# Optimization experiments

Measured on AMD Instinct MI355X. Metric: run time of the kernel, lower is better.

Reference implementation:

```python
import jax, jax.numpy as jnp
import numpy as np

N, B, E, H, G, L = 128, 2, 512, 1024, 50, 3
RBF_RADIUS = 12.0
AVG_LEN = 60.0


def _resmlp(h, Win, bin_, Wh, bh, Wout, bout):
    # input proj + activation, residual hidden blocks, linear head
    h = jax.nn.gelu(h @ Win + bin_, approximate=False)
    for i in range(Wh.shape[0]):  # fixed small number of layers
        h = h + jax.nn.gelu(h @ Wh[i] + bh[i], approximate=False)
    return h @ Wout + bout


def setup_inputs() -> dict:
    key = jax.random.key(0)
    ks = jax.random.split(key, 20)
    s_in = 1.0 / np.sqrt(3 * E)
    s_h = 1.0 / np.sqrt(H)
    s_g = 1.0 / np.sqrt(G)
    return {
        'x': jax.random.normal(ks[0], (N, B, E), jnp.float32),
        'dist': jax.random.uniform(ks[1], (N, N, B), jnp.float32),
        'vec_hat': jax.random.normal(ks[2], (N, N, B, 3), jnp.float32),
        'mask': jnp.ones((B, N), dtype=bool),
        'rbf_W': jax.random.normal(ks[3], (G, E), jnp.float32) * s_g,
        'rbf_b': jnp.zeros((E,), jnp.float32),
        'e_Win': jax.random.normal(ks[4], (3 * E, H), jnp.float32) * s_in,
        'e_bin': jnp.zeros((H,), jnp.float32),
        'e_Wh': jax.random.normal(ks[5], (L, H, H), jnp.float32) * s_h,
        'e_bh': jnp.zeros((L, H), jnp.float32),
        'e_Wout': jax.random.normal(ks[6], (H, 1), jnp.float32) * s_h,
        'e_bout': jnp.zeros((1,), jnp.float32),
        'f_Win': jax.random.normal(ks[7], (3 * E, H), jnp.float32) * s_in,
        'f_bin': jnp.zeros((H,), jnp.float32),
        'f_Wh': jax.random.normal(ks[8], (L, H, H), jnp.float32) * s_h,
        'f_bh': jnp.zeros((L, H), jnp.float32),
        'f_Wout': jax.random.normal(ks[9], (H, 1), jnp.float32) * s_h,
        'f_bout': jnp.zeros((1,), jnp.float32),
    }


def reference(x, dist, vec_hat, mask, rbf_W, rbf_b, e_Win, e_bin, e_Wh, e_bh,
              e_Wout, e_bout, f_Win, f_bin, f_Wh, f_bh, f_Wout, f_bout):
    # Gaussian RBF expansion + linear projection to embed_dim
    offset = jnp.linspace(0.0, RBF_RADIUS, G)
    coeff = -0.5 / (offset[1] - offset[0]) ** 2
    g = jnp.exp(coeff * (dist[..., None] - offset) ** 2)       # (N,N,B,G)
    rbf = g @ rbf_W + rbf_b                                    # (N,N,B,E)

    # all-pairs concat feature: [x_i, x_j, rbf_ij]  -> (N,N,B,3E)
    feat = jnp.concatenate([
        jnp.broadcast_to(x[:, None], rbf.shape),
        jnp.broadcast_to(x[None, :], rbf.shape),
        rbf,
    ], axis=-1)

    entries = (mask.T[:, None] & mask.T[None, :])[..., None].astype(feat.dtype)  # (N,N,B,1)

    energy_pairs = _resmlp(feat, e_Win, e_bin, e_Wh, e_bh, e_Wout, e_bout)       # (N,N,B,1)
    force_pairs = _resmlp(feat, f_Win, f_bin, f_Wh, f_bh, f_Wout, f_bout) * vec_hat  # (N,N,B,3)

    energy = (energy_pairs * entries).sum((0, 1)) / AVG_LEN ** 2  # (B,1)
    forces = (force_pairs * entries).sum(0) / AVG_LEN             # (N,B,3)
    # torch: forces.transpose(0,1)[mask]; mask is all-True here, so this is a reshape
    forces = jnp.swapaxes(forces, 0, 1).reshape(-1, 3)            # (B*N,3)
    return energy, forces
```

## Files before the change

### kernel.cpp

```cpp
#include <hip/hip_runtime.h>
#include <stdint.h>

typedef __bf16 bf16x8 __attribute__((ext_vector_type(8)));
typedef __bf16 bf16x4 __attribute__((ext_vector_type(4)));
typedef float  f32x4  __attribute__((ext_vector_type(4)));
typedef unsigned int u32;

__device__ __forceinline__ void gl_lds16(const void* gptr, void* lptr) {
    __builtin_amdgcn_global_load_lds(
        (const __attribute__((address_space(1))) u32*)gptr,
        (__attribute__((address_space(3))) u32*)lptr,
        16, 0, 0);
}

__device__ __forceinline__ float gelu_f(float x) {
    float u = 0.7978845608f * x * (1.0f + 0.044715f * x * x);
    float e = __expf(2.0f * u);
    float t = 1.0f - 2.0f / (e + 1.0f);
    return 0.5f * x * (1.0f + t);
}

#define MEMFENCE __asm__ __volatile__("" ::: "memory")

__global__ __launch_bounds__(256)
void prep_all(const float* __restrict__ dist, __bf16* __restrict__ G,
              const float* __restrict__ x, __bf16* __restrict__ xb,
              const float* __restrict__ rbfW, const float* __restrict__ rbf_b,
              __bf16* __restrict__ M1, float* __restrict__ out) {
    const int b = blockIdx.x;
    const int t = threadIdx.x;
    if (b < 1024) {
        const int row = b * 32 + (t >> 3);
        const int c0 = (t & 7) * 8;
        const float sp = 12.0f / 49.0f;
        const float coeff = -0.5f / (sp * sp);
        const float d = dist[row];
        bf16x8 v;
#pragma unroll
        for (int q = 0; q < 8; ++q) {
            const int k = c0 + q;
            float val;
            if (k < 50)       { float tt = d - (float)k * sp; val = __expf(coeff * tt * tt); }
            else if (k == 50) val = 1.0f;
            else              val = 0.0f;
            v[q] = (__bf16)val;
        }
        *(bf16x8*)(G + (size_t)row * 64 + c0) = v;
    } else if (b < 1152) {
        const int idx = (b - 1024) * 256 + t;
        float4 v = *(const float4*)(x + idx * 4);
        bf16x4 o;
        o[0] = (__bf16)v.x; o[1] = (__bf16)v.y; o[2] = (__bf16)v.z; o[3] = (__bf16)v.w;
        *(bf16x4*)(xb + idx * 4) = o;
    } else if (b < 1280) {
        const int tt = (b - 1152) * 256 + t;
        const int r = tt >> 8;
        const int c = (tt & 255) * 2;
        float v0 = 0.f, v1 = 0.f;
        if (r < 50)       { v0 = rbfW[r * 512 + c]; v1 = rbfW[r * 512 + c + 1]; }
        else if (r == 50) { v0 = rbf_b[c];          v1 = rbf_b[c + 1]; }
        M1[r * 512 + c] = (__bf16)v0;
        M1[r * 512 + c + 1] = (__bf16)v1;
    } else {
        const int i = (b - 1280) * 256 + t;
        if (i < 770) out[i] = 0.0f;
    }
}

__global__ __launch_bounds__(256)
void transpose_all(const float* __restrict__ eWin, const float* __restrict__ fWin,
                   __bf16* __restrict__ eWinT, __bf16* __restrict__ fWinT,
                   const float* __restrict__ eWh, const float* __restrict__ fWh,
                   __bf16* __restrict__ eWhT, __bf16* __restrict__ fWhT) {
    const int z = blockIdx.z;
    int K, branch, l;
    const float* src;
    __bf16* dst;
    if (z < 2) {
        K = 1536; branch = z; l = 0;
        src = branch ? fWin : eWin;
        dst = branch ? fWinT : eWinT;
    } else {
        K = 1024; const int zz = z - 2; branch = zz / 3; l = zz - branch * 3;
        src = (branch ? fWh : eWh) + (size_t)l * 1024 * 1024;
        dst = (branch ? fWhT : eWhT) + (size_t)l * 1024 * 1024;
    }
    const int Ncols = 1024;
    const int bk = blockIdx.x * 64;
    if (bk >= K) return;
    const int bn = blockIdx.y * 64;

    __shared__ float tile[64][65];
    const int tid = threadIdx.x;
    const int tr = tid >> 4;
    const int tc = (tid & 15) * 4;
#pragma unroll
    for (int p = 0; p < 4; ++p) {
        const int r = tr + p * 16;
        float4 v = *(const float4*)&src[(size_t)(bk + r) * Ncols + bn + tc];
        tile[r][tc] = v.x; tile[r][tc + 1] = v.y;
        tile[r][tc + 2] = v.z; tile[r][tc + 3] = v.w;
    }
    __syncthreads();
#pragma unroll
    for (int p = 0; p < 4; ++p) {
        const int rn = tr + p * 16;
        bf16x4 o;
        o[0] = (__bf16)tile[tc + 0][rn];
        o[1] = (__bf16)tile[tc + 1][rn];
        o[2] = (__bf16)tile[tc + 2][rn];
        o[3] = (__bf16)tile[tc + 3][rn];
        *(bf16x4*)&dst[(size_t)(bn + rn) * K + bk + tc] = o;
    }
}

template <int NK, int NBN, int MODE, bool DUAL, int MINW, bool SWZ>
__global__ __launch_bounds__(256, MINW)
void gemm_k(const __bf16* __restrict__ A0, const __bf16* __restrict__ A1,
            const __bf16* __restrict__ B0, const __bf16* __restrict__ B1,
            int lda, int ldb, int ldc,
            const float* __restrict__ bias0, const float* __restrict__ bias1,
            __bf16* __restrict__ C0, __bf16* __restrict__ C1,
            float* __restrict__ Cf0, float* __restrict__ Cf1,
            const float* __restrict__ P0, const float* __restrict__ P1,
            const float* __restrict__ wout0, const float* __restrict__ wout1,
            float* __restrict__ dot0, float* __restrict__ dot1) {
    constexpr int NBS = (NBN == 16) ? 4 : (NBN == 8) ? 3 : 0;
    __shared__ __align__(16) __bf16 As[3][128 * 32];
    __shared__ __align__(16) __bf16 Bs[3][128 * 32];

    const int tid = threadIdx.x;
    int bn, bm, branch = 0;
    if constexpr (SWZ) {
        const int x = blockIdx.x & 7;
        const int slot = blockIdx.x >> 3;
        bn = slot & (NBN - 1);
        int grp = x + ((slot >> NBS) << 3);
        if constexpr (DUAL) {
            const int half = (gridDim.x >> NBS) >> 1;
            branch = (grp >= half);
            if (branch) grp -= half;
        }
        bm = grp;
    } else {
        int f2 = blockIdx.x;
        if constexpr (DUAL) {
            const int half = gridDim.x >> 1;
            branch = (f2 >= half);
            if (branch) f2 -= half;
        }
        bn = f2 & (NBN - 1);
        bm = f2 >> NBS;
    }
    const int w = tid >> 6;
    const int lane = tid & 63;

    const __bf16* Ab = (DUAL && branch) ? A1 : A0;
    const __bf16* Bb = (DUAL && branch) ? B1 : B0;

    const int r0 = tid >> 2;
    const int s0 = tid & 3;
    const char* gA0 = (const char*)Ab + (size_t)(bm * 128 + r0) * lda + s0 * 16;
    const char* gA1 = gA0 + (size_t)64 * lda;
    const char* gB0 = (const char*)Bb + (size_t)(bn * 128 + r0) * ldb + s0 * 16;
    const char* gB1 = gB0 + (size_t)64 * ldb;

    char* lA0 = (char*)&As[0][0] + w * 1024;
    char* lA1 = (char*)&As[1][0] + w * 1024;
    char* lA2 = (char*)&As[2][0] + w * 1024;
    char* lB0 = (char*)&Bs[0][0] + w * 1024;
    char* lB1 = (char*)&Bs[1][0] + w * 1024;
    char* lB2 = (char*)&Bs[2][0] + w * 1024;

    const int wm = (w >> 1) & 1;
    const int wn = w & 1;
    const int lm = lane & 15;
    const int ko = (lane >> 4) << 3;
    const int fo = (wm * 64 + lm) * 32 + ko;
    const int go = (wn * 64 + lm) * 32 + ko;
    const __bf16* pA0 = &As[0][0] + fo;
    const __bf16* pA1 = &As[1][0] + fo;
    const __bf16* pA2 = &As[2][0] + fo;
    const __bf16* pB0 = &Bs[0][0] + go;
    const __bf16* pB1 = &Bs[1][0] + go;
    const __bf16* pB2 = &Bs[2][0] + go;

    f32x4 acc[4][4];
    const f32x4 zero = {0.0f, 0.0f, 0.0f, 0.0f};
#pragma unroll
    for (int i = 0; i < 4; ++i)
#pragma unroll
        for (int j = 0; j < 4; ++j) acc[i][j] = zero;

    auto stage = [&](int buf) {
        char* la = (buf == 0) ? lA0 : (buf == 1) ? lA1 : lA2;
        char* lb = (buf == 0) ? lB0 : (buf == 1) ? lB1 : lB2;
        gl_lds16(gA0, la); gl_lds16(gA1, la + 4096);
        gl_lds16(gB0, lb); gl_lds16(gB1, lb + 4096);
        gA0 += 64; gA1 += 64; gB0 += 64; gB1 += 64;
    };
    auto compute = [&](int buf) {
        const __bf16* pa = (buf == 0) ? pA0 : (buf == 1) ? pA1 : pA2;
        const __bf16* pb = (buf == 0) ? pB0 : (buf == 1) ? pB1 : pB2;
        bf16x8 af[4], bfg[4];
#pragma unroll
        for (int i = 0; i < 4; ++i) {
            af[i]  = *(const bf16x8*)(pa + i * 512);
            bfg[i] = *(const bf16x8*)(pb + i * 512);
        }
#pragma unroll
        for (int mi = 0; mi < 4; ++mi)
#pragma unroll
            for (int ni = 0; ni < 4; ++ni)
                acc[mi][ni] = __builtin_amdgcn_mfma_f32_16x16x32_bf16(
                    af[mi], bfg[ni], acc[mi][ni], 0, 0, 0);
    };
    auto iterstep = [&](int cbuf, int sbuf) {
        MEMFENCE;
        __builtin_amdgcn_s_waitcnt(0xF74);
        __builtin_amdgcn_s_barrier();
        MEMFENCE;
        compute(cbuf);
        MEMFENCE;
        stage(sbuf);
        MEMFENCE;
    };

    stage(0);
    stage(1);
    constexpr int NIT = NK - 2;
    constexpr int NG = NIT / 3;
    constexpr int NR = NIT % 3;
    for (int g = 0; g < NG; ++g) {
        iterstep(0, 2);
        iterstep(1, 0);
        iterstep(2, 1);
    }
    if constexpr (NR >= 1) iterstep(0, 2);
    if constexpr (NR >= 2) iterstep(1, 0);
    MEMFENCE;
    __builtin_amdgcn_s_waitcnt(0xF74);
    __builtin_amdgcn_s_barrier();
    MEMFENCE;
    compute((NK - 2) % 3);
    MEMFENCE;
    __builtin_amdgcn_s_waitcnt(0xF70);
    __builtin_amdgcn_s_barrier();
    MEMFENCE;
    compute((NK - 1) % 3);

    const int col0 = bn * 128 + wn * 64 + lm;
    const int row0 = bm * 128 + wm * 64 + ((lane >> 4) << 2);
    const int ldaE = lda >> 1;

    float rowdot[16];
    if constexpr (MODE == 1) {
#pragma unroll
        for (int q = 0; q < 16; ++q) rowdot[q] = 0.0f;
    }

    const bool side = (MODE == 2) && (bn >= 8);
    const float* bp = (MODE == 2) ? (side ? bias1 : bias0)
                                  : ((DUAL && branch) ? bias1 : bias0);
    __bf16* Cout = (MODE == 2) ? (side ? C1 : C0)
                               : ((DUAL && branch) ? C1 : C0);
    const float* woutb = (MODE == 1) ? ((DUAL && branch) ? wout1 : wout0) : nullptr;

#pragma unroll
    for (int ni = 0; ni < 4; ++ni) {
        const int gn = col0 + ni * 16;
        const int gnl = (MODE == 2) ? (gn & 1023) : gn;
        float bv = 0.0f;
        if constexpr (MODE <= 2) bv = bp[gnl];
        float wv = 0.0f;
        if constexpr (MODE == 1) wv = woutb[gn];

        float res[16];
        if constexpr (MODE == 0 || MODE == 1) {
#pragma unroll
            for (int mi = 0; mi < 4; ++mi)
#pragma unroll
                for (int rr = 0; rr < 4; ++rr)
                    res[mi * 4 + rr] =
                        (float)Ab[(size_t)(row0 + mi * 16 + rr) * ldaE + gn];
        } else if constexpr (MODE == 2) {
#pragma unroll
            for (int mi = 0; mi < 4; ++mi)
#pragma unroll
                for (int rr = 0; rr < 4; ++rr) {
                    const int gm = row0 + mi * 16 + rr;
                    const int p0row = ((gm >> 8) << 1) | (gm & 1);
                    const int p1row = gm & 255;
                    res[mi * 4 + rr] = P0[(size_t)p0row * 2048 + gn]
                                     + P1[(size_t)p1row * 2048 + gn];
                }
        }
        MEMFENCE;

#pragma unroll
        for (int mi = 0; mi < 4; ++mi) {
#pragma unroll
            for (int rr = 0; rr < 4; ++rr) {
                const int gm = row0 + mi * 16 + rr;
                const float a = acc[mi][ni][rr];
                if constexpr (MODE == 0) {
                    float v = gelu_f(a + bv) + res[mi * 4 + rr];
                    Cout[(size_t)gm * ldc + gn] = (__bf16)v;
                } else if constexpr (MODE == 1) {
                    float v = gelu_f(a + bv) + res[mi * 4 + rr];
                    rowdot[mi * 4 + rr] += v * wv;
                } else if constexpr (MODE == 2) {
                    float v = a + bv + res[mi * 4 + rr];
                    Cout[(size_t)gm * ldc + gnl] = (__bf16)gelu_f(v);
                } else if constexpr (MODE == 3) {
                    float* Cfw = (DUAL && branch) ? Cf1 : Cf0;
                    Cfw[(size_t)gm * ldc + gn] = a;
                } else {
                    C0[(size_t)gm * ldc + gn] = (__bf16)a;
                }
            }
        }
    }

    if constexpr (MODE == 1) {
#pragma unroll
        for (int s = 1; s < 16; s <<= 1)
#pragma unroll
            for (int q = 0; q < 16; ++q) rowdot[q] += __shfl_xor(rowdot[q], s);
        if (lm == 0) {
            float* dotb = (DUAL && branch) ? dot1 : dot0;
            float* dp = dotb + (size_t)(bn * 2 + wn) * 32768 + row0;
#pragma unroll
            for (int q = 0; q < 16; ++q)
                dp[(q >> 2) * 16 + (q & 3)] = rowdot[q];
        }
    }
}

#define WBAR(imm) do { MEMFENCE; __builtin_amdgcn_s_waitcnt(imm); \
                       __builtin_amdgcn_s_barrier(); MEMFENCE; } while (0)

template <int MODE, bool DUAL, int NBN, int NT, int LDA, int LDB>
__global__ __launch_bounds__(256, 2)
void gemm256(const __bf16* __restrict__ A0, const __bf16* __restrict__ A1,
             const __bf16* __restrict__ B0, const __bf16* __restrict__ B1,
             const float* __restrict__ bias0, const float* __restrict__ bias1,
             __bf16* __restrict__ C0, __bf16* __restrict__ C1,
             const float* __restrict__ wout0, const float* __restrict__ wout1,
             float* __restrict__ dot0, float* __restrict__ dot1,
             const float* __restrict__ P0, const float* __restrict__ P1) {
    constexpr int NBS = (NBN == 16) ? 4 : (NBN == 8) ? 3 : 2;
    __shared__ __align__(16) char ldsbuf[2 * 24576];

    const int tid = threadIdx.x;
    const int nxg = gridDim.x >> 3;
    const int id = (blockIdx.x & 7) * nxg + (blockIdx.x >> 3);
    const int bn = id & (NBN - 1);
    int rest = id >> NBS;
    int branch = 0;
    if constexpr (DUAL) { branch = rest >> 7; rest &= 127; }
    const int bm = rest;

    const __bf16* __restrict__ Ab = (DUAL && branch) ? A1 : A0;
    const __bf16* __restrict__ Bb = (DUAL && branch) ? B1 : B0;

    const int w = tid >> 6;
    const int lane = tid & 63;

    const int srow = tid >> 2;
    const int scol = ((tid & 3) << 4) ^ (((tid >> 3) & 3) << 4);
    const char* gA = (const char*)Ab + (size_t)(bm * 256 + srow) * LDA + scol;
    const char* gB = (const char*)Bb + (size_t)(bn * 128 + srow) * LDB + scol;

    auto stageT = [&](int kt, int buf) {
        const size_t ko = (size_t)kt * 64;
        char* d = ldsbuf + buf * 24576 + w * 1024;
        gl_lds16(gA + ko,             d);
        gl_lds16(gA + ko +  64 * LDA, d + 4096);
        gl_lds16(gA + ko + 128 * LDA, d + 8192);
        gl_lds16(gA + ko + 192 * LDA, d + 12288);
        gl_lds16(gB + ko,             d + 16384);
        gl_lds16(gB + ko +  64 * LDB, d + 20480);
    };

    const int wm = w >> 1, wn = w & 1;
    const int lm = lane & 15, lq = lane >> 4;
    const int swz = ((lm >> 1) & 3) << 4;
    const int rA = (wm * 128 + lm) * 64 + ((lq * 16) ^ swz);
    const int rB = 16384 + (wn * 64 + lm) * 64 + ((lq * 16) ^ swz);

    f32x4 acc[4][8];
    const f32x4 zero = {0.0f, 0.0f, 0.0f, 0.0f};
#pragma unroll
    for (int i = 0; i < 4; ++i)
#pragma unroll
        for (int j = 0; j < 8; ++j) acc[i][j] = zero;

    auto body2 = [&](int kt, int buf, bool dostage) {
        const char* Lb = ldsbuf + buf * 24576;
        MEMFENCE;
        bf16x8 a[8], b[4];
#pragma unroll
        for (int ni = 0; ni < 4; ++ni)
            b[ni] = *(const bf16x8*)(Lb + rB + ni * 1024);
#pragma unroll
        for (int mi = 0; mi < 8; ++mi)
            a[mi] = *(const bf16x8*)(Lb + rA + mi * 1024);
        MEMFENCE;
        __builtin_amdgcn_s_waitcnt(0xC07F);
        MEMFENCE;
        __builtin_amdgcn_s_barrier();
        MEMFENCE;
        if (dostage) stageT(kt + 2, buf);
        MEMFENCE;
        __builtin_amdgcn_s_setprio(1);
#pragma unroll
        for (int ni = 0; ni < 4; ++ni)
#pragma unroll
            for (int mi = 0; mi < 8; ++mi)
                acc[ni][mi] = __builtin_amdgcn_mfma_f32_16x16x32_bf16(
                    b[ni], a[mi], acc[ni][mi], 0, 0, 0);
        __builtin_amdgcn_s_setprio(0);
    };

    if constexpr (NT == 32) {
        stageT(0, 0);
        stageT(1, 1);
        for (int g = 0; g < 15; ++g) {
            WBAR(0xF76); body2(2 * g + 0, 0, true);
            WBAR(0xF76); body2(2 * g + 1, 1, true);
        }
        WBAR(0xF76); body2(30, 0, false);
        WBAR(0xF70); body2(31, 1, false);
    } else {
        stageT(0, 0);
        stageT(1, 1);
        WBAR(0xF76); body2(0, 0, false);
        WBAR(0xF70); body2(1, 1, false);
    }

    const int rowb = bm * 256 + wm * 128 + lm;
    const int nbase = bn * 128 + wn * 64 + lq * 4;

    if constexpr (MODE == 2) {
        const bool side = (bn >= (NBN >> 1));
        const float* __restrict__ bp = side ? bias1 : bias0;
        __bf16* __restrict__ Cw = side ? C1 : C0;
        const int nloc = nbase & 1023;
        f32x4 bv[4], p0v[4];
        const size_t p0base = (size_t)((bm << 1) | (lm & 1)) * 2048;
#pragma unroll
        for (int ni = 0; ni < 4; ++ni) {
            bv[ni]  = *(const f32x4*)&bp[nloc + ni * 16];
            p0v[ni] = *(const f32x4*)&P0[p0base + nbase + ni * 16];
        }
#pragma unroll
        for (int mi = 0; mi < 8; ++mi) {
            const int p1row = wm * 128 + mi * 16 + lm;
            f32x4 p1v[4];
#pragma unroll
            for (int ni = 0; ni < 4; ++ni)
                p1v[ni] = *(const f32x4*)&P1[(size_t)p1row * 2048 + nbase + ni * 16];
            MEMFENCE;
            const size_t rb = (size_t)(rowb + mi * 16) * 1024;
#pragma unroll
            for (int ni = 0; ni < 4; ++ni) {
                bf16x4 o;
#pragma unroll
                for (int r = 0; r < 4; ++r)
                    o[r] = (__bf16)gelu_f(acc[ni][mi][r] + bv[ni][r] +
                                          p0v[ni][r] + p1v[ni][r]);
                *(bf16x4*)&Cw[rb + nloc + ni * 16] = o;
            }
        }
        return;
    }

    const float* __restrict__ bp = (DUAL && branch) ? bias1 : bias0;
    f32x4 bv[4];
#pragma unroll
    for (int ni = 0; ni < 4; ++ni)
        bv[ni] = *(const f32x4*)&bp[nbase + ni * 16];

    if constexpr (MODE == 0) {
        __bf16* __restrict__ Cw = (DUAL && branch) ? C1 : C0;
#pragma unroll
        for (int mi = 0; mi < 8; ++mi) {
            const size_t rb = (size_t)(rowb + mi * 16) * 1024;
            bf16x4 res[4];
#pragma unroll
            for (int ni = 0; ni < 4; ++ni)
                res[ni] = *(const bf16x4*)&Ab[rb + nbase + ni * 16];
            MEMFENCE;
#pragma unroll
            for (int ni = 0; ni < 4; ++ni) {
                bf16x4 o;
#pragma unroll
                for (int r = 0; r < 4; ++r)
                    o[r] = (__bf16)(gelu_f(acc[ni][mi][r] + bv[ni][r]) +
                                    (float)res[ni][r]);
                *(bf16x4*)&Cw[rb + nbase + ni * 16] = o;
            }
        }
    } else if constexpr (MODE == 1) {
        const float* __restrict__ wb = (DUAL && branch) ? wout1 : wout0;
        f32x4 wv[4];
#pragma unroll
        for (int ni = 0; ni < 4; ++ni)
            wv[ni] = *(const f32x4*)&wb[nbase + ni * 16];
        float rd[8];
#pragma unroll
        for (int q = 0; q < 8; ++q) rd[q] = 0.0f;
#pragma unroll
        for (int mi = 0; mi < 8; ++mi) {
            const size_t rb = (size_t)(rowb + mi * 16) * 1024;
            bf16x4 res[4];
#pragma unroll
            for (int ni = 0; ni < 4; ++ni)
                res[ni] = *(const bf16x4*)&Ab[rb + nbase + ni * 16];
            MEMFENCE;
#pragma unroll
            for (int ni = 0; ni < 4; ++ni)
#pragma unroll
                for (int r = 0; r < 4; ++r) {
                    float v = gelu_f(acc[ni][mi][r] + bv[ni][r]) +
                              (float)res[ni][r];
                    rd[mi] += v * wv[ni][r];
                }
        }
#pragma unroll
        for (int mi = 0; mi < 8; ++mi) {
            rd[mi] += __shfl_xor(rd[mi], 16);
            rd[mi] += __shfl_xor(rd[mi], 32);
        }
        if (lq == 0) {
            float* __restrict__ db = (DUAL && branch) ? dot1 : dot0;
            float* dp = db + (size_t)(bn * 2 + wn) * 32768 + bm * 256 + wm * 128;
#pragma unroll
            for (int mi = 0; mi < 8; ++mi)
                dp[mi * 16 + lm] = rd[mi];
        }
    }
}

__global__ __launch_bounds__(128)
void finalize(const float* __restrict__ dot_e, const float* __restrict__ dot_f,
              const float* __restrict__ eb, const float* __restrict__ fb,
              const float* __restrict__ vec, float* __restrict__ out) {
    const int bj = blockIdx.x;
    const int bb = bj >> 7, jj = bj & 127;
    const int i = threadIdx.x;
    const int m = (i * 128 + jj) * 2 + bb;
    float e = eb[0], f = fb[0];
#pragma unroll
    for (int s = 0; s < 16; ++s) {
        e += dot_e[(size_t)s * 32768 + m];
        f += dot_f[(size_t)s * 32768 + m];
    }
    f *= (1.0f / 60.0f);
    float fx = f * vec[(size_t)m * 3 + 0];
    float fy = f * vec[(size_t)m * 3 + 1];
    float fz = f * vec[(size_t)m * 3 + 2];
#pragma unroll
    for (int off = 32; off > 0; off >>= 1) {
        e  += __shfl_down(e, off);
        fx += __shfl_down(fx, off);
        fy += __shfl_down(fy, off);
        fz += __shfl_down(fz, off);
    }
    __shared__ float red[2][4];
    const int wv = i >> 6, lane = i & 63;
    if (lane == 0) { red[wv][0] = e; red[wv][1] = fx; red[wv][2] = fy; red[wv][3] = fz; }
    __syncthreads();
    if (i == 0) {
        atomicAdd(&out[bb], (red[0][0] + red[1][0]) * (1.0f / 3600.0f));
        float* fo = out + 2 + bj * 3;
        fo[0] = red[0][1] + red[1][1];
        fo[1] = red[0][2] + red[1][2];
        fo[2] = red[0][3] + red[1][3];
    }
}

extern "C" void kernel_launch(void* const* d_in, const int* in_sizes, int n_in,
                              void* d_out, int out_size, void* d_ws, size_t ws_size,
                              hipStream_t stream) {
    const float* x     = (const float*)d_in[0];
    const float* dist  = (const float*)d_in[1];
    const float* vec   = (const float*)d_in[2];
    const float* rbfW  = (const float*)d_in[4];
    const float* rbf_b = (const float*)d_in[5];
    const float* eWin  = (const float*)d_in[6];
    const float* ebin  = (const float*)d_in[7];
    const float* eWh   = (const float*)d_in[8];
    const float* ebh   = (const float*)d_in[9];
    const float* eWout = (const float*)d_in[10];
    const float* ebout = (const float*)d_in[11];
    const float* fWin  = (const float*)d_in[12];
    const float* fbin  = (const float*)d_in[13];
    const float* fWh   = (const float*)d_in[14];
    const float* fbh   = (const float*)d_in[15];
    const float* fWout = (const float*)d_in[16];
    const float* fbout = (const float*)d_in[17];
    float* out = (float*)d_out;

    char* p = (char*)d_ws;
    __bf16* WinTcat = (__bf16*)p;
    __bf16* eWinT = WinTcat;          p += (size_t)1024 * 1536 * 2;
    __bf16* fWinT = (__bf16*)p;       p += (size_t)1024 * 1536 * 2;
    __bf16* eWhT0 = (__bf16*)p;       p += (size_t)3 * 1024 * 1024 * 2;
    __bf16* fWhT0 = (__bf16*)p;       p += (size_t)3 * 1024 * 1024 * 2;
    __bf16* xb  = (__bf16*)p;         p += (size_t)256 * 512 * 2;
    __bf16* M1  = (__bf16*)p;         p += (size_t)128 * 512 * 2;
    __bf16* WgT = (__bf16*)p;         p += (size_t)2048 * 128 * 2;
    __bf16* G   = (__bf16*)p;         p += (size_t)32768 * 64 * 2;
    float* P0   = (float*)p;          p += (size_t)256 * 2048 * 4;
    float* P1   = (float*)p;          p += (size_t)256 * 2048 * 4;
    float* dot_e = (float*)p;         p += (size_t)16 * 32768 * 4;
    float* dot_f = (float*)p;         p += (size_t)16 * 32768 * 4;
    const size_t SLAB = (size_t)32768 * 1024 * 2;
    __bf16* he0 = (__bf16*)p;         p += SLAB;
    __bf16* hf0 = (__bf16*)p;         p += SLAB;
    __bf16* hA  = (__bf16*)p;         p += SLAB;

    prep_all<<<dim3(1284), dim3(256), 0, stream>>>(
        dist, G, x, xb, rbfW, rbf_b, M1, out);
    transpose_all<<<dim3(24, 16, 8), dim3(256), 0, stream>>>(
        eWin, fWin, eWinT, fWinT, eWh, fWh, eWhT0, fWhT0);

    const dim3 blk(256);
    gemm_k<16, 16, 3, true, 3, false><<<dim3(64), blk, 0, stream>>>(
        xb, xb, WinTcat, WinTcat + 512, 1024, 3072, 2048,
        nullptr, nullptr, nullptr, nullptr, P0, P1,
        nullptr, nullptr, nullptr, nullptr, nullptr, nullptr);
    gemm_k<16, 1, 4, false, 3, false><<<dim3(16), blk, 0, stream>>>(
        WinTcat + 1024, nullptr, M1, nullptr, 3072, 1024, 128,
        nullptr, nullptr, WgT, nullptr, nullptr, nullptr,
        nullptr, nullptr, nullptr, nullptr, nullptr, nullptr);

    gemm256<2, false, 16, 2, 128, 256><<<dim3(2048), blk, 0, stream>>>(
        G, nullptr, WgT, nullptr, ebin, fbin, he0, hf0,
        nullptr, nullptr, nullptr, nullptr, P0, P1);

    gemm256<0, false, 8, 32, 2048, 2048><<<dim3(1024), blk, 0, stream>>>(
        he0, nullptr, eWhT0, nullptr, ebh + 0, nullptr,
        hA, nullptr, nullptr, nullptr, nullptr, nullptr, nullptr, nullptr);
    gemm256<0, false, 8, 32, 2048, 2048><<<dim3(1024), blk, 0, stream>>>(
        hA, nullptr, eWhT0 + (size_t)1048576, nullptr, ebh + 1024, nullptr,
        he0, nullptr, nullptr, nullptr, nullptr, nullptr, nullptr, nullptr);
    gemm256<0, false, 8, 32, 2048, 2048><<<dim3(1024), blk, 0, stream>>>(
        hf0, nullptr, fWhT0, nullptr, fbh + 0, nullptr,
        hA, nullptr, nullptr, nullptr, nullptr, nullptr, nullptr, nullptr);
    gemm256<0, false, 8, 32, 2048, 2048><<<dim3(1024), blk, 0, stream>>>(
        hA, nullptr, fWhT0 + (size_t)1048576, nullptr, fbh + 1024, nullptr,
        hf0, nullptr, nullptr, nullptr, nullptr, nullptr, nullptr, nullptr);
    gemm256<1, true, 8, 32, 2048, 2048><<<dim3(2048), blk, 0, stream>>>(
        he0, hf0, eWhT0 + (size_t)2 * 1048576, fWhT0 + (size_t)2 * 1048576,
        ebh + 2048, fbh + 2048, nullptr, nullptr,
        eWout, fWout, dot_e, dot_f, nullptr, nullptr);

    finalize<<<dim3(256), dim3(128), 0, stream>>>(dot_e, dot_f, ebout, fbout, vec, out);
}
```

Measured before the change: 693.9 us.

## Load hidden-layer weights directly into registers from MFMA-fragment-packed layout

The transpose kernel now writes hidden-layer weight matrices (z>=2) in a pre-swizzled layout that matches the per-lane MFMA B-fragment order. The 256-row GEMMs for the hidden layers then load B straight from global memory into registers, double-buffered one tile ahead, and stage only A through LDS. This drops the B LDS traffic and halves the B portion of shared memory, which could raise occupancy. In exchange, B loads now travel through the vector memory path with more registers held live, and the wait-count immediates are adjusted for fewer outstanding LDS-DMA ops.

```diff
diff --git a/kernel.cpp b/kernel.cpp
--- a/kernel.cpp
+++ b/kernel.cpp
@@ -110,7 +110,16 @@
         o[1] = (__bf16)tile[tc + 1][rn];
         o[2] = (__bf16)tile[tc + 2][rn];
         o[3] = (__bf16)tile[tc + 3][rn];
-        *(bf16x4*)&dst[(size_t)(bn + rn) * K + bk + tc] = o;
+        if (z < 2) {
+            *(bf16x4*)&dst[(size_t)(bn + rn) * K + bk + tc] = o;
+        } else {
+            const int n = bn + rn, k0 = bk + tc;
+            const size_t off =
+                (size_t)((n >> 4) * 32 + (k0 >> 5)) * 1024 +
+                (size_t)((n & 15) | (((k0 >> 3) & 3) << 4)) * 16 +
+                (size_t)(k0 & 7) * 2;
+            *(bf16x4*)((char*)dst + off) = o;
+        }
     }
 }
 
@@ -340,7 +349,7 @@
 #define WBAR(imm) do { MEMFENCE; __builtin_amdgcn_s_waitcnt(imm); \
                        __builtin_amdgcn_s_barrier(); MEMFENCE; } while (0)
 
-template <int MODE, bool DUAL, int NBN, int NT, int LDA, int LDB>
+template <int MODE, bool DUAL, int NBN, int NT, int LDA, int LDB, bool BD>
 __global__ __launch_bounds__(256, 2)
 void gemm256(const __bf16* __restrict__ A0, const __bf16* __restrict__ A1,
              const __bf16* __restrict__ B0, const __bf16* __restrict__ B1,
@@ -350,7 +359,8 @@
              float* __restrict__ dot0, float* __restrict__ dot1,
              const float* __restrict__ P0, const float* __restrict__ P1) {
     constexpr int NBS = (NBN == 16) ? 4 : (NBN == 8) ? 3 : 2;
-    __shared__ __align__(16) char ldsbuf[2 * 24576];
+    constexpr int BUFSZ = BD ? 16384 : 24576;
+    __shared__ __align__(16) char ldsbuf[2 * BUFSZ];
 
     const int tid = threadIdx.x;
     const int nxg = gridDim.x >> 3;
@@ -372,9 +382,17 @@
     const char* gA = (const char*)Ab + (size_t)(bm * 256 + srow) * LDA + scol;
     const char* gB = (const char*)Bb + (size_t)(bn * 128 + srow) * LDB + scol;
 
+    auto stageA4 = [&](int kt, int buf) {
+        const size_t ko = (size_t)kt * 64;
+        char* d = ldsbuf + buf * BUFSZ + w * 1024;
+        gl_lds16(gA + ko,             d);
+        gl_lds16(gA + ko +  64 * LDA, d + 4096);
+        gl_lds16(gA + ko + 128 * LDA, d + 8192);
+        gl_lds16(gA + ko + 192 * LDA, d + 12288);
+    };
     auto stageT = [&](int kt, int buf) {
         const size_t ko = (size_t)kt * 64;
-        char* d = ldsbuf + buf * 24576 + w * 1024;
+        char* d = ldsbuf + buf * BUFSZ + w * 1024;
         gl_lds16(gA + ko,             d);
         gl_lds16(gA + ko +  64 * LDA, d + 4096);
         gl_lds16(gA + ko + 128 * LDA, d + 8192);
@@ -389,6 +407,12 @@
     const int rA = (wm * 128 + lm) * 64 + ((lq * 16) ^ swz);
     const int rB = 16384 + (wn * 64 + lm) * 64 + ((lq * 16) ^ swz);
 
+    const char* pB[4];
+#pragma unroll
+    for (int ni = 0; ni < 4; ++ni)
+        pB[ni] = (const char*)Bb +
+                 (size_t)(bn * 8 + wn * 4 + ni) * 32768 + (size_t)lane * 16;
+
     f32x4 acc[4][8];
     const f32x4 zero = {0.0f, 0.0f, 0.0f, 0.0f};
 #pragma unroll
@@ -396,8 +420,41 @@
 #pragma unroll
         for (int j = 0; j < 8; ++j) acc[i][j] = zero;
 
+    bf16x8 b0[4], b1[4];
+    auto loadB = [&](int kt, bf16x8* bb) {
+        MEMFENCE;
+#pragma unroll
+        for (int ni = 0; ni < 4; ++ni)
+            bb[ni] = *(const bf16x8*)(pB[ni] + (size_t)kt * 1024);
+        MEMFENCE;
+    };
+
+    auto bodyBD = [&](int kt, int buf, bf16x8* bcur, bool dostage) {
+        const char* Lb = ldsbuf + buf * BUFSZ;
+        MEMFENCE;
+        bf16x8 a[8];
+#pragma unroll
+        for (int mi = 0; mi < 8; ++mi)
+            a[mi] = *(const bf16x8*)(Lb + rA + mi * 1024);
+        MEMFENCE;
+        __builtin_amdgcn_s_waitcnt(0xC07F);
+        MEMFENCE;
+        __builtin_amdgcn_s_barrier();
+        MEMFENCE;
+        if (dostage) stageA4(kt + 2, buf);
+        MEMFENCE;
+        __builtin_amdgcn_s_setprio(1);
+#pragma unroll
+        for (int ni = 0; ni < 4; ++ni)
+#pragma unroll
+            for (int mi = 0; mi < 8; ++mi)
+                acc[ni][mi] = __builtin_amdgcn_mfma_f32_16x16x32_bf16(
+                    bcur[ni], a[mi], acc[ni][mi], 0, 0, 0);
+        __builtin_amdgcn_s_setprio(0);
+    };
+
     auto body2 = [&](int kt, int buf, bool dostage) {
-        const char* Lb = ldsbuf + buf * 24576;
+        const char* Lb = ldsbuf + buf * BUFSZ;
         MEMFENCE;
         bf16x8 a[8], b[4];
 #pragma unroll
@@ -423,16 +480,18 @@
         __builtin_amdgcn_s_setprio(0);
     };
 
-    if constexpr (NT == 32) {
-        stageT(0, 0);
-        stageT(1, 1);
+    if constexpr (NT == 32 && BD) {
+        stageA4(0, 0); loadB(0, b0);
+        stageA4(1, 1); loadB(1, b1);
         for (int g = 0; g < 15; ++g) {
-            WBAR(0xF76); body2(2 * g + 0, 0, true);
-            WBAR(0xF76); body2(2 * g + 1, 1, true);
-        }
-        WBAR(0xF76); body2(30, 0, false);
-        WBAR(0xF70); body2(31, 1, false);
-    } else {
+            WBAR(0xF78);
+            bodyBD(2 * g + 0, 0, b0, true); loadB(2 * g + 2, b0);
+            WBAR(0xF78);
+            bodyBD(2 * g + 1, 1, b1, true); loadB(2 * g + 3, b1);
+        }
+        WBAR(0xF78); bodyBD(30, 0, b0, false);
+        WBAR(0xF70); bodyBD(31, 1, b1, false);
+    } else if constexpr (NT == 2) {
         stageT(0, 0);
         stageT(1, 1);
         WBAR(0xF76); body2(0, 0, false);
@@ -637,23 +696,23 @@
         nullptr, nullptr, WgT, nullptr, nullptr, nullptr,
         nullptr, nullptr, nullptr, nullptr, nullptr, nullptr);
 
-    gemm256<2, false, 16, 2, 128, 256><<<dim3(2048), blk, 0, stream>>>(
+    gemm256<2, false, 16, 2, 128, 256, false><<<dim3(2048), blk, 0, stream>>>(
         G, nullptr, WgT, nullptr, ebin, fbin, he0, hf0,
         nullptr, nullptr, nullptr, nullptr, P0, P1);
 
-    gemm256<0, false, 8, 32, 2048, 2048><<<dim3(1024), blk, 0, stream>>>(
+    gemm256<0, false, 8, 32, 2048, 2048, true><<<dim3(1024), blk, 0, stream>>>(
         he0, nullptr, eWhT0, nullptr, ebh + 0, nullptr,
         hA, nullptr, nullptr, nullptr, nullptr, nullptr, nullptr, nullptr);
-    gemm256<0, false, 8, 32, 2048, 2048><<<dim3(1024), blk, 0, stream>>>(
+    gemm256<0, false, 8, 32, 2048, 2048, true><<<dim3(1024), blk, 0, stream>>>(
         hA, nullptr, eWhT0 + (size_t)1048576, nullptr, ebh + 1024, nullptr,
         he0, nullptr, nullptr, nullptr, nullptr, nullptr, nullptr, nullptr);
-    gemm256<0, false, 8, 32, 2048, 2048><<<dim3(1024), blk, 0, stream>>>(
+    gemm256<0, false, 8, 32, 2048, 2048, true><<<dim3(1024), blk, 0, stream>>>(
         hf0, nullptr, fWhT0, nullptr, fbh + 0, nullptr,
         hA, nullptr, nullptr, nullptr, nullptr, nullptr, nullptr, nullptr);
-    gemm256<0, false, 8, 32, 2048, 2048><<<dim3(1024), blk, 0, stream>>>(
+    gemm256<0, false, 8, 32, 2048, 2048, true><<<dim3(1024), blk, 0, stream>>>(
         hA, nullptr, fWhT0 + (size_t)1048576, nullptr, fbh + 1024, nullptr,
         hf0, nullptr, nullptr, nullptr, nullptr, nullptr, nullptr, nullptr);
-    gemm256<1, true, 8, 32, 2048, 2048><<<dim3(2048), blk, 0, stream>>>(
+    gemm256<1, true, 8, 32, 2048, 2048, true><<<dim3(2048), blk, 0, stream>>>(
         he0, hf0, eWhT0 + (size_t)2 * 1048576, fWhT0 + (size_t)2 * 1048576,
         ebh + 2048, fbh + 2048, nullptr, nullptr,
         eWout, fWout, dot_e, dot_f, nullptr, nullptr);
```

Measured after the change: 688.1 us, median of 2. About the same (-0.8%).
